# Kernel optimization log

Hardware: AMD Instinct MI355X
Metric: run time of the kernel (lower is better)

The kernel has to match this reference:

```python
import jax, jax.numpy as jnp
import numpy as np

FILTERS = [1, 3, 7, 9]
BN_EPS = 1e-5


def _conv1d(x, w, b):
    # x: [B, C, L], w: [O, I, F] (torch Conv1d layout), 'same' padding for odd F
    pad = (w.shape[-1] - 1) // 2
    y = jax.lax.conv_general_dilated(
        x, w, window_strides=(1,), padding=[(pad, pad)],
        dimension_numbers=("NCH", "OIH", "NCH"))
    return y + b[None, :, None]


def _bn_elu(x, gamma, beta):
    # BatchNorm1d in training mode: biased batch stats over (batch, length)
    m = jnp.mean(x, axis=(0, 2), keepdims=True)
    v = jnp.var(x, axis=(0, 2), keepdims=True)
    xn = (x - m) * jax.lax.rsqrt(v + BN_EPS)
    return jax.nn.elu(xn * gamma[None, :, None] + beta[None, :, None])


def setup_inputs() -> dict:
    key = jax.random.key(0)
    ks = jax.random.split(key, 32)
    b, h, l, lk, dk = 8, 8, 1024, 1024, 64
    inp = {
        "Q": jax.random.normal(ks[0], (b, h, l, dk), jnp.float32),
        "K": jax.random.normal(ks[1], (b, h, lk, dk), jnp.float32),
        "V": jax.random.normal(ks[2], (b, h, lk, dk), jnp.float32),
        "W_pq": jax.random.normal(ks[3], (1, dk), jnp.float32) * 0.1,
        "W_bq": jax.random.normal(ks[4], (dk, 1), jnp.float32) * 0.1,
        "W_bk": jax.random.normal(ks[5], (dk, 1), jnp.float32) * 0.1,
        "bn_g": jax.random.uniform(ks[6], (h,), jnp.float32, 0.5, 1.5),
        "bn_b": jax.random.normal(ks[7], (h,), jnp.float32) * 0.1,
        "attn_mask": jnp.ones((1,), dtype=bool),
    }
    for i, f in enumerate(FILTERS):
        s = 1.0 / np.sqrt(h * f)
        inp[f"cq_w{i}"] = jax.random.normal(ks[8 + i], (h, h, f), jnp.float32) * s
        inp[f"cq_b{i}"] = jax.random.normal(ks[12 + i], (h,), jnp.float32) * 0.05
        inp[f"ck_w{i}"] = jax.random.normal(ks[16 + i], (h, h, f), jnp.float32) * s
        inp[f"ck_b{i}"] = jax.random.normal(ks[20 + i], (h,), jnp.float32) * 0.05
    return inp


def reference(Q, K, V, W_pq, W_bq, W_bk,
              cq_w0, cq_b0, cq_w1, cq_b1, cq_w2, cq_b2, cq_w3, cq_b3,
              ck_w0, ck_b0, ck_w1, ck_b1, ck_w2, ck_b2, ck_w3, ck_b3,
              bn_g, bn_b, attn_mask):
    b, h, l, dk = Q.shape
    lk = K.shape[2]
    nf = len(FILTERS)
    # proj_q applied to BOTH Q and K (proj_k is dead in the original code)
    q = jnp.einsum("bhld,d->bhl", Q, W_pq[0])  # [b,h,l]
    k = jnp.einsum("bhld,d->bhl", K, W_pq[0])  # [b,h,lk]
    cq = [(cq_w0, cq_b0), (cq_w1, cq_b1), (cq_w2, cq_b2), (cq_w3, cq_b3)]
    ck = [(ck_w0, ck_b0), (ck_w1, ck_b1), (ck_w2, ck_b2), (ck_w3, ck_b3)]
    Q_l = [_bn_elu(_conv1d(q, w, bb), bn_g, bn_b) for w, bb in cq]
    K_l = [_bn_elu(_conv1d(k, w, bb), bn_g, bn_b) for w, bb in ck]
    # replicate torch.cat(dim=0) + reshape(b,h,nf*len) flat-order semantics
    Q_p = jnp.concatenate(Q_l, axis=0).reshape(b, h, nf * l)    # [b,h,4l]
    K_p = jnp.concatenate(K_l, axis=0).reshape(b, h, nf * lk)   # [b,h,4lk]
    Qt = jax.lax.top_k(Q_p, l)[0]                               # [b,h,l]
    Km = jnp.mean(K_p.reshape(b, h, nf, lk), axis=2)            # [b,h,lk]
    Kt = jax.lax.top_k(Km, lk)[0]                               # descending sort
    Qb = Qt[..., None] * W_bq[:, 0]                             # [b,h,l,dk]
    Kb = Kt[..., None] * W_bk[:, 0]                             # [b,h,lk,dk]
    scores = jnp.einsum("bhqd,bhkd->bhqk", Qb, Kb) / np.float32(np.sqrt(dk))
    attn = jax.nn.softmax(scores, axis=-1)
    context = jnp.einsum("bhqk,bhkd->bhqd", attn, V)
    return context, attn
```

## Files before the change

kernel.cpp:

```cpp
#include <hip/hip_runtime.h>
#include <hip/hip_bf16.h>
#include <math.h>

namespace {
constexpr int PROJ_OFF = 0;
constexpr int CONV_OFF = 131072;
constexpr int PS_OFF   = 655360;
constexpr int PSS_OFF  = 657408;
constexpr int QT_OFF   = 659456;
constexpr int KT_OFF   = 724992;

typedef short bf16x8 __attribute__((ext_vector_type(8)));
typedef float f32x4 __attribute__((ext_vector_type(4)));

union BF8 {
  bf16x8 v;
  short s[8];
};

__global__ __launch_bounds__(256) void proj_kernel(
    const float* __restrict__ Q, const float* __restrict__ K,
    const float* __restrict__ Wpq, float* __restrict__ proj) {
  __shared__ float wsh[64];
  const int tid = threadIdx.x;
  if (tid < 64) wsh[tid] = Wpq[tid];
  __syncthreads();
  const int row = blockIdx.x * 256 + tid;
  const float* src = (row < 65536) ? (Q + (size_t)row * 64)
                                   : (K + (size_t)(row - 65536) * 64);
  float acc = 0.f;
#pragma unroll
  for (int j = 0; j < 16; ++j) {
    const float4 v = *(const float4*)(src + j * 4);
    acc = fmaf(v.x, wsh[j * 4 + 0], acc);
    acc = fmaf(v.y, wsh[j * 4 + 1], acc);
    acc = fmaf(v.z, wsh[j * 4 + 2], acc);
    acc = fmaf(v.w, wsh[j * 4 + 3], acc);
  }
  proj[row] = acc;
}

template <int F>
__device__ void conv_body(const float* __restrict__ xs,
                          const float* __restrict__ wsm,
                          const float* __restrict__ bsm,
                          float* __restrict__ outp, int tid, int lq,
                          float accs[8]) {
  constexpr int pad = (F - 1) / 2;
#pragma unroll
  for (int j = 0; j < 8; ++j) {
    float acc = bsm[j];
#pragma unroll
    for (int c = 0; c < 8; ++c) {
      const float* xrow = &xs[c * 264 + tid + 4 - pad];
      const float* wrow = &wsm[(j * 8 + c) * F];
#pragma unroll
      for (int f = 0; f < F; ++f) acc = fmaf(xrow[f], wrow[f], acc);
    }
    outp[j * 1024 + lq * 256 + tid] = acc;
    accs[j] = acc;
  }
}

__global__ __launch_bounds__(256) void conv_kernel(
    const float* __restrict__ proj,
    const float* __restrict__ wq0, const float* __restrict__ bq0,
    const float* __restrict__ wq1, const float* __restrict__ bq1,
    const float* __restrict__ wq2, const float* __restrict__ bq2,
    const float* __restrict__ wq3, const float* __restrict__ bq3,
    const float* __restrict__ wk0, const float* __restrict__ bk0,
    const float* __restrict__ wk1, const float* __restrict__ bk1,
    const float* __restrict__ wk2, const float* __restrict__ bk2,
    const float* __restrict__ wk3, const float* __restrict__ bk3,
    float* __restrict__ conv, float* __restrict__ psum,
    float* __restrict__ psumsq) {
  __shared__ float xs[8 * 264];
  __shared__ float wsm[8 * 8 * 9];
  __shared__ float bsm[8];
  __shared__ float redS[8][4], redSS[8][4];
  const int tid = threadIdx.x;
  const int blk = blockIdx.x;
  const int path = blk >> 7, fi = (blk >> 5) & 3, bb = (blk >> 2) & 7;
  const int lq = blk & 3;
  const int F = (0x9731 >> (fi * 4)) & 0xF;
  const float* wp;
  const float* bp;
  if (path == 0) {
    wp = fi == 0 ? wq0 : fi == 1 ? wq1 : fi == 2 ? wq2 : wq3;
    bp = fi == 0 ? bq0 : fi == 1 ? bq1 : fi == 2 ? bq2 : bq3;
  } else {
    wp = fi == 0 ? wk0 : fi == 1 ? wk1 : fi == 2 ? wk2 : wk3;
    bp = fi == 0 ? bk0 : fi == 1 ? bk1 : fi == 2 ? bk2 : bk3;
  }
  const float* pb = proj + path * 65536 + bb * 8192;
  for (int e = tid; e < 8 * 264; e += 256) {
    const int c = e / 264, pos = e - c * 264;
    const int gl = lq * 256 + pos - 4;
    xs[e] = (gl >= 0 && gl < 1024) ? pb[c * 1024 + gl] : 0.f;
  }
  for (int e = tid; e < 64 * F; e += 256) wsm[e] = wp[e];
  if (tid < 8) bsm[tid] = bp[tid];
  __syncthreads();
  float* outp = conv + ((size_t)(path * 4 + fi) * 8 + bb) * 8192;
  float accs[8];
  if (fi == 0)
    conv_body<1>(xs, wsm, bsm, outp, tid, lq, accs);
  else if (fi == 1)
    conv_body<3>(xs, wsm, bsm, outp, tid, lq, accs);
  else if (fi == 2)
    conv_body<7>(xs, wsm, bsm, outp, tid, lq, accs);
  else
    conv_body<9>(xs, wsm, bsm, outp, tid, lq, accs);
  const int lane = tid & 63, wv = tid >> 6;
#pragma unroll
  for (int j = 0; j < 8; ++j) {
    float sv = accs[j], qv = accs[j] * accs[j];
#pragma unroll
    for (int mm = 32; mm >= 1; mm >>= 1) {
      sv += __shfl_xor(sv, mm, 64);
      qv += __shfl_xor(qv, mm, 64);
    }
    if (lane == 0) {
      redS[j][wv] = sv;
      redSS[j][wv] = qv;
    }
  }
  __syncthreads();
  if (tid < 16) {
    const int j = tid & 7;
    const bool wantss = tid >= 8;
    const float* rr = wantss ? &redSS[j][0] : &redS[j][0];
    const float tot = rr[0] + rr[1] + rr[2] + rr[3];
    float* dst = wantss ? psumsq : psum;
    dst[((path * 4 + fi) * 8 + j) * 32 + bb * 4 + lq] = tot;
  }
}

__device__ inline float bn_elu(float v, float mean, float rstd, float g,
                               float be) {
  const float x = (v - mean) * rstd * g + be;
  return x > 0.f ? x : expm1f(x);
}

__device__ inline void cswap(float& a, float& b, bool up) {
  const float mx = fmaxf(a, b), mn = fminf(a, b);
  a = up ? mx : mn;
  b = up ? mn : mx;
}

__device__ inline void shfl_pass(float v[4], int t, int m, bool up) {
  const bool keepmax = (up == ((t & m) == 0));
#pragma unroll
  for (int e = 0; e < 4; ++e) {
    const float p = __shfl_xor(v[e], m, 64);
    v[e] = keepmax ? fmaxf(v[e], p) : fminf(v[e], p);
  }
}

__device__ inline void lds_pass(float v[4], float* s, int t, int jq, bool up) {
  *(float4*)&s[4 * t] = make_float4(v[0], v[1], v[2], v[3]);
  __syncthreads();
  const int pt = t ^ jq;
  const bool keepmax = (up == ((t & jq) == 0));
  const float4 p = *(const float4*)&s[4 * pt];
  v[0] = keepmax ? fmaxf(v[0], p.x) : fminf(v[0], p.x);
  v[1] = keepmax ? fmaxf(v[1], p.y) : fminf(v[1], p.y);
  v[2] = keepmax ? fmaxf(v[2], p.z) : fminf(v[2], p.z);
  v[3] = keepmax ? fmaxf(v[3], p.w) : fminf(v[3], p.w);
  __syncthreads();
}

__device__ inline void reg_tail(float v[4], int t, bool up) {
#pragma unroll
  for (int m = 32; m >= 1; m >>= 1) shfl_pass(v, t, m, up);
  cswap(v[0], v[2], up);
  cswap(v[1], v[3], up);
  cswap(v[0], v[1], up);
  cswap(v[2], v[3], up);
}

__device__ inline void sort1024(float v[4], float* s, int t) {
  cswap(v[0], v[1], true);
  cswap(v[2], v[3], false);
#pragma unroll
  for (int k = 4; k <= 256; k <<= 1) {
    const bool up = ((t & (k >> 2)) == 0);
    for (int m = k >> 3; m >= 1; m >>= 1) shfl_pass(v, t, m, up);
    cswap(v[0], v[2], up);
    cswap(v[1], v[3], up);
    cswap(v[0], v[1], up);
    cswap(v[2], v[3], up);
  }
  {
    const bool up = ((t & 128) == 0);
    lds_pass(v, s, t, 64, up);
    reg_tail(v, t, up);
  }
  lds_pass(v, s, t, 128, true);
  lds_pass(v, s, t, 64, true);
  reg_tail(v, t, true);
}

__device__ inline void bmerge1024(float v[4], float* s, int t) {
  lds_pass(v, s, t, 128, true);
  lds_pass(v, s, t, 64, true);
  reg_tail(v, t, true);
}

__global__ __launch_bounds__(256) void sortmerge_kernel(
    const float* __restrict__ conv, const float* __restrict__ psum,
    const float* __restrict__ psumsq, const float* __restrict__ bng,
    const float* __restrict__ bnb, float* __restrict__ Qt,
    float* __restrict__ Kt) {
  __shared__ float s[1024];
  __shared__ float sred[8];
  __shared__ float cm[4], cr[4];
  const int t = threadIdx.x, blk = blockIdx.x;
  const bool isQ = blk < 64;
  const int row = isQ ? blk : blk - 64;
  const int hp = row & 7;
  const int fi = row >> 4;
  const int bb = ((row >> 3) & 1) * 4 + (hp >> 1);
  const int chbase = (isQ ? 0 : 32) + fi * 8 + (hp & 1) * 4;
  if (t < 8) {
    const float* src = (t < 4) ? psum : psumsq;
    const int ch = chbase + (t & 3);
    float a = 0.f;
    for (int i = 0; i < 32; ++i) a += src[ch * 32 + i];
    sred[t] = a;
  }
  __syncthreads();
  if (t < 4) {
    const float mean = sred[t] * (1.f / 8192.f);
    const float var = sred[4 + t] * (1.f / 8192.f) - mean * mean;
    cm[t] = mean;
    cr[t] = rsqrtf(fmaxf(var, 0.f) + 1e-5f);
  }
  __syncthreads();
  if (isQ) {
    const float* base = conv + (size_t)(fi * 8 + bb) * 8192;
    float c0[4], c1[4], c2[4], c3[4];
#pragma unroll
    for (int jc = 0; jc < 4; ++jc) {
      float* v = jc == 0 ? c0 : jc == 1 ? c1 : jc == 2 ? c2 : c3;
      const int hh = (hp & 1) * 4 + jc;
      const float mean = cm[jc], rstd = cr[jc];
      const float g = bng[hh], be = bnb[hh];
      const float4 x = *(const float4*)&base[hh * 1024 + 4 * t];
      v[0] = bn_elu(x.x, mean, rstd, g, be);
      v[1] = bn_elu(x.y, mean, rstd, g, be);
      v[2] = bn_elu(x.z, mean, rstd, g, be);
      v[3] = bn_elu(x.w, mean, rstd, g, be);
      sort1024(v, s, t);
    }
    float a[4], b[4];
    *(float4*)&s[4 * t] = make_float4(c1[0], c1[1], c1[2], c1[3]);
    __syncthreads();
#pragma unroll
    for (int e = 0; e < 4; ++e) a[e] = fmaxf(c0[e], s[1023 - 4 * t - e]);
    __syncthreads();
    bmerge1024(a, s, t);
    *(float4*)&s[4 * t] = make_float4(c3[0], c3[1], c3[2], c3[3]);
    __syncthreads();
#pragma unroll
    for (int e = 0; e < 4; ++e) b[e] = fmaxf(c2[e], s[1023 - 4 * t - e]);
    __syncthreads();
    bmerge1024(b, s, t);
    *(float4*)&s[4 * t] = make_float4(b[0], b[1], b[2], b[3]);
    __syncthreads();
#pragma unroll
    for (int e = 0; e < 4; ++e) a[e] = fmaxf(a[e], s[1023 - 4 * t - e]);
    __syncthreads();
    bmerge1024(a, s, t);
    *(float4*)&Qt[(size_t)row * 1024 + 4 * t] =
        make_float4(a[0], a[1], a[2], a[3]);
  } else {
    float v[4];
    float sum0 = 0.f, sum1 = 0.f, sum2 = 0.f, sum3 = 0.f;
#pragma unroll
    for (int j = 0; j < 4; ++j) {
      const int hh = (hp & 1) * 4 + j;
      const float mean = cm[j], rstd = cr[j];
      const float g = bng[hh], be = bnb[hh];
      const float4 x = *(const float4*)&conv[(size_t)(4 + fi) * 64 * 1024 +
                                             (size_t)bb * 8192 + hh * 1024 +
                                             4 * t];
      sum0 += bn_elu(x.x, mean, rstd, g, be);
      sum1 += bn_elu(x.y, mean, rstd, g, be);
      sum2 += bn_elu(x.z, mean, rstd, g, be);
      sum3 += bn_elu(x.w, mean, rstd, g, be);
    }
    v[0] = sum0 * 0.25f;
    v[1] = sum1 * 0.25f;
    v[2] = sum2 * 0.25f;
    v[3] = sum3 * 0.25f;
    sort1024(v, s, t);
    *(float4*)&Kt[(size_t)row * 1024 + 4 * t] =
        make_float4(v[0], v[1], v[2], v[3]);
  }
}

__global__ __launch_bounds__(256, 4) void attn5_kernel(
    const float* __restrict__ V, const float* __restrict__ Qt,
    const float* __restrict__ Kt, const float* __restrict__ Wbq,
    const float* __restrict__ Wbk, float* __restrict__ ctx,
    float* __restrict__ attn) {
  __shared__ float Kts[1024];
  __shared__ float sq[64], mq[64], rz[64];
  __shared__ short Vhi[2][8 * 64 * 8];
  __shared__ short Vlo[2][8 * 64 * 8];
  const int tid = threadIdx.x;
  const int b = blockIdx.x;
  const int bh = ((b & 7) << 3) | ((b >> 3) & 7);
  const int qt = b >> 6;
  const int qbase = qt * 64;
  const int lane0 = tid & 63;
  float cval;
  {
    float d = Wbq[lane0] * Wbk[lane0];
#pragma unroll
    for (int mm = 32; mm >= 1; mm >>= 1) d += __shfl_xor(d, mm, 64);
    cval = d * 0.125f;
  }
  const float* Ktg = Kt + (size_t)bh * 1024;
  for (int t = tid; t < 1024; t += 256) Kts[t] = Ktg[t];
  const float kHi = Ktg[0], kLo = Ktg[1023];
  if (tid < 64) {
    const float s = cval * Qt[(size_t)bh * 1024 + qbase + tid];
    sq[tid] = s;
    mq[tid] = fmaxf(s * kHi, s * kLo);
  }
  __syncthreads();
  {
    const int row = tid >> 2, qtr = tid & 3;
    const float s = sq[row], m = mq[row];
    float z = 0.f;
    const int k0 = qtr * 256;
    for (int k = 0; k < 256; ++k) z += __expf(fmaf(s, Kts[k0 + k], -m));
    z += __shfl_xor(z, 1, 64);
    z += __shfl_xor(z, 2, 64);
    if (qtr == 0) rz[row] = 1.f / z;
  }
  __syncthreads();

  const int wv = tid >> 6, l = tid & 63;
  const int l15 = l & 15, l4 = l >> 4;
  const int q = wv * 16 + l15;
  const float s = sq[q], m = mq[q], r = rz[q];
  f32x4 acc[4];
#pragma unroll
  for (int dt = 0; dt < 4; ++dt) acc[dt] = (f32x4){0.f, 0.f, 0.f, 0.f};

  const float* Vb = V + (size_t)bh * 65536;
  float* arow = attn + ((size_t)bh << 20) + (size_t)qbase * 1024;
  const int dV = tid & 63, kqV = tid >> 6;

  for (int ch = 0; ch < 16; ++ch) {
    const int kc = ch * 64;
    const int buf = ch & 1;
    float vreg[2][8];
#pragma unroll
    for (int g = 0; g < 2; ++g) {
      const int ko = kqV + g * 4;
      const float* vs = Vb + (size_t)(kc + ko * 8) * 64 + dV;
#pragma unroll
      for (int i = 0; i < 8; ++i) vreg[g][i] = vs[i * 64];
    }
    bf16x8 ahi[2], alo[2];
#pragma unroll
    for (int ks = 0; ks < 2; ++ks) {
      const int kb = kc + ks * 32 + l4 * 8;
      const float4 kv0 = *(const float4*)&Kts[kb];
      const float4 kv1 = *(const float4*)&Kts[kb + 4];
      float e[8];
      e[0] = __expf(fmaf(s, kv0.x, -m)) * r;
      e[1] = __expf(fmaf(s, kv0.y, -m)) * r;
      e[2] = __expf(fmaf(s, kv0.z, -m)) * r;
      e[3] = __expf(fmaf(s, kv0.w, -m)) * r;
      e[4] = __expf(fmaf(s, kv1.x, -m)) * r;
      e[5] = __expf(fmaf(s, kv1.y, -m)) * r;
      e[6] = __expf(fmaf(s, kv1.z, -m)) * r;
      e[7] = __expf(fmaf(s, kv1.w, -m)) * r;
      float* ag = arow + (size_t)q * 1024 + kb;
      *(float4*)ag = make_float4(e[0], e[1], e[2], e[3]);
      *(float4*)(ag + 4) = make_float4(e[4], e[5], e[6], e[7]);
      BF8 H, L;
#pragma unroll
      for (int i = 0; i < 8; ++i) {
        const __hip_bfloat16 hb = __float2bfloat16(e[i]);
        H.s[i] = __bfloat16_as_short(hb);
        L.s[i] =
            __bfloat16_as_short(__float2bfloat16(e[i] - __bfloat162float(hb)));
      }
      ahi[ks] = H.v;
      alo[ks] = L.v;
    }
#pragma unroll
    for (int g = 0; g < 2; ++g) {
      const int ko = kqV + g * 4;
      BF8 H, L;
#pragma unroll
      for (int i = 0; i < 8; ++i) {
        const float f = vreg[g][i];
        const __hip_bfloat16 hb = __float2bfloat16(f);
        H.s[i] = __bfloat16_as_short(hb);
        L.s[i] =
            __bfloat16_as_short(__float2bfloat16(f - __bfloat162float(hb)));
      }
      *(bf16x8*)&Vhi[buf][(ko * 64 + dV) * 8] = H.v;
      *(bf16x8*)&Vlo[buf][(ko * 64 + dV) * 8] = L.v;
    }
    __syncthreads();
#pragma unroll
    for (int ks = 0; ks < 2; ++ks) {
      const int ko = ks * 4 + l4;
#pragma unroll
      for (int dt = 0; dt < 4; ++dt) {
        const bf16x8 bhv =
            *(const bf16x8*)&Vhi[buf][(ko * 64 + dt * 16 + l15) * 8];
        const bf16x8 blv =
            *(const bf16x8*)&Vlo[buf][(ko * 64 + dt * 16 + l15) * 8];
        acc[dt] = __builtin_amdgcn_mfma_f32_16x16x32_bf16(ahi[ks], bhv,
                                                          acc[dt], 0, 0, 0);
        acc[dt] = __builtin_amdgcn_mfma_f32_16x16x32_bf16(ahi[ks], blv,
                                                          acc[dt], 0, 0, 0);
        acc[dt] = __builtin_amdgcn_mfma_f32_16x16x32_bf16(alo[ks], bhv,
                                                          acc[dt], 0, 0, 0);
      }
    }
  }
  float* cb = ctx + ((size_t)bh * 1024 + qbase + wv * 16 + l4 * 4) * 64 + l15;
#pragma unroll
  for (int dt = 0; dt < 4; ++dt)
#pragma unroll
    for (int rr = 0; rr < 4; ++rr) cb[(size_t)rr * 64 + dt * 16] = acc[dt][rr];
}

}

extern "C" void kernel_launch(void* const* d_in, const int* in_sizes, int n_in,
                              void* d_out, int out_size, void* d_ws,
                              size_t ws_size, hipStream_t stream) {
  const float* Q = (const float*)d_in[0];
  const float* K = (const float*)d_in[1];
  const float* V = (const float*)d_in[2];
  const float* Wpq = (const float*)d_in[3];
  const float* Wbq = (const float*)d_in[4];
  const float* Wbk = (const float*)d_in[5];
  const float* bng = (const float*)d_in[6];
  const float* bnb = (const float*)d_in[7];
  const float* cqw[4] = {(const float*)d_in[9], (const float*)d_in[13],
                         (const float*)d_in[17], (const float*)d_in[21]};
  const float* cqb[4] = {(const float*)d_in[10], (const float*)d_in[14],
                         (const float*)d_in[18], (const float*)d_in[22]};
  const float* ckw[4] = {(const float*)d_in[11], (const float*)d_in[15],
                         (const float*)d_in[19], (const float*)d_in[23]};
  const float* ckb[4] = {(const float*)d_in[12], (const float*)d_in[16],
                         (const float*)d_in[20], (const float*)d_in[24]};

  float* ws = (float*)d_ws;
  float* proj = ws + PROJ_OFF;
  float* conv = ws + CONV_OFF;
  float* psum = ws + PS_OFF;
  float* psumsq = ws + PSS_OFF;
  float* Qtp = ws + QT_OFF;
  float* Ktp = ws + KT_OFF;
  float* ctx = (float*)d_out;
  float* attn = ctx + (size_t)8 * 8 * 1024 * 64;

  proj_kernel<<<512, 256, 0, stream>>>(Q, K, Wpq, proj);
  conv_kernel<<<256, 256, 0, stream>>>(
      proj, cqw[0], cqb[0], cqw[1], cqb[1], cqw[2], cqb[2], cqw[3], cqb[3],
      ckw[0], ckb[0], ckw[1], ckb[1], ckw[2], ckb[2], ckw[3], ckb[3], conv,
      psum, psumsq);
  sortmerge_kernel<<<128, 256, 0, stream>>>(conv, psum, psumsq, bng, bnb, Qtp,
                                            Ktp);
  attn5_kernel<<<1024, 256, 0, stream>>>(V, Qtp, Ktp, Wbq, Wbk, ctx, attn);
}
```

Baseline: 119.8 us.

## Process 128 query rows per block to reuse V conversion across two tiles

The attention kernel now handles 128 queries per block instead of 64, and the grid is halved. Each wave computes two 16-row MFMA tiles that share the same bf16 hi/lo V tiles in LDS, so V loads and splits are amortised over twice as many queries. The softmax normaliser is folded into the exponent as -m-log(z), which removes a multiply per element. The attn row stores are moved after a custom lgkmcnt barrier so they overlap with the MFMA phase. In exchange, register pressure roughly doubles (launch bounds drop to 2 blocks per SM), and only 512 blocks remain to fill the GPU.

```diff
diff --git a/kernel.cpp b/kernel.cpp
--- a/kernel.cpp
+++ b/kernel.cpp
@@ -17,6 +17,13 @@
   bf16x8 v;
   short s[8];
 };
+
+__device__ inline void lgkm_barrier() {
+  __builtin_amdgcn_sched_barrier(0);
+  asm volatile("s_waitcnt lgkmcnt(0)" ::: "memory");
+  __builtin_amdgcn_s_barrier();
+  __builtin_amdgcn_sched_barrier(0);
+}
 
 __global__ __launch_bounds__(256) void proj_kernel(
     const float* __restrict__ Q, const float* __restrict__ K,
@@ -300,20 +307,20 @@
   }
 }
 
-__global__ __launch_bounds__(256, 4) void attn5_kernel(
+__global__ __launch_bounds__(256, 2) void attn6_kernel(
     const float* __restrict__ V, const float* __restrict__ Qt,
     const float* __restrict__ Kt, const float* __restrict__ Wbq,
     const float* __restrict__ Wbk, float* __restrict__ ctx,
     float* __restrict__ attn) {
   __shared__ float Kts[1024];
-  __shared__ float sq[64], mq[64], rz[64];
+  __shared__ float sq[128], cz[128];
   __shared__ short Vhi[2][8 * 64 * 8];
   __shared__ short Vlo[2][8 * 64 * 8];
   const int tid = threadIdx.x;
   const int b = blockIdx.x;
   const int bh = ((b & 7) << 3) | ((b >> 3) & 7);
   const int qt = b >> 6;
-  const int qbase = qt * 64;
+  const int qbase = qt * 128;
   const int lane0 = tid & 63;
   float cval;
   {
@@ -325,31 +332,37 @@
   const float* Ktg = Kt + (size_t)bh * 1024;
   for (int t = tid; t < 1024; t += 256) Kts[t] = Ktg[t];
   const float kHi = Ktg[0], kLo = Ktg[1023];
-  if (tid < 64) {
+  __shared__ float msh[128];
+  if (tid < 128) {
     const float s = cval * Qt[(size_t)bh * 1024 + qbase + tid];
     sq[tid] = s;
-    mq[tid] = fmaxf(s * kHi, s * kLo);
+    msh[tid] = fmaxf(s * kHi, s * kLo);
   }
   __syncthreads();
   {
-    const int row = tid >> 2, qtr = tid & 3;
-    const float s = sq[row], m = mq[row];
+    const int row = tid >> 1, half = tid & 1;
+    const float s = sq[row], m = msh[row];
+    const int k0 = half * 512;
     float z = 0.f;
-    const int k0 = qtr * 256;
-    for (int k = 0; k < 256; ++k) z += __expf(fmaf(s, Kts[k0 + k], -m));
+    for (int k = 0; k < 512; ++k) z += __expf(fmaf(s, Kts[k0 + k], -m));
     z += __shfl_xor(z, 1, 64);
-    z += __shfl_xor(z, 2, 64);
-    if (qtr == 0) rz[row] = 1.f / z;
+    if (half == 0) cz[row] = -m - __logf(z);
   }
   __syncthreads();
 
   const int wv = tid >> 6, l = tid & 63;
   const int l15 = l & 15, l4 = l >> 4;
-  const int q = wv * 16 + l15;
-  const float s = sq[q], m = mq[q], r = rz[q];
-  f32x4 acc[4];
-#pragma unroll
-  for (int dt = 0; dt < 4; ++dt) acc[dt] = (f32x4){0.f, 0.f, 0.f, 0.f};
+  float s_[2], c_[2];
+#pragma unroll
+  for (int t = 0; t < 2; ++t) {
+    s_[t] = sq[wv * 32 + t * 16 + l15];
+    c_[t] = cz[wv * 32 + t * 16 + l15];
+  }
+  f32x4 acc[2][4];
+#pragma unroll
+  for (int t = 0; t < 2; ++t)
+#pragma unroll
+    for (int dt = 0; dt < 4; ++dt) acc[t][dt] = (f32x4){0.f, 0.f, 0.f, 0.f};
 
   const float* Vb = V + (size_t)bh * 65536;
   float* arow = attn + ((size_t)bh << 20) + (size_t)qbase * 1024;
@@ -366,34 +379,38 @@
 #pragma unroll
       for (int i = 0; i < 8; ++i) vreg[g][i] = vs[i * 64];
     }
-    bf16x8 ahi[2], alo[2];
+    bf16x8 ahi[2][2], alo[2][2];
+    float4 est[2][2][2];
 #pragma unroll
     for (int ks = 0; ks < 2; ++ks) {
       const int kb = kc + ks * 32 + l4 * 8;
       const float4 kv0 = *(const float4*)&Kts[kb];
       const float4 kv1 = *(const float4*)&Kts[kb + 4];
-      float e[8];
-      e[0] = __expf(fmaf(s, kv0.x, -m)) * r;
-      e[1] = __expf(fmaf(s, kv0.y, -m)) * r;
-      e[2] = __expf(fmaf(s, kv0.z, -m)) * r;
-      e[3] = __expf(fmaf(s, kv0.w, -m)) * r;
-      e[4] = __expf(fmaf(s, kv1.x, -m)) * r;
-      e[5] = __expf(fmaf(s, kv1.y, -m)) * r;
-      e[6] = __expf(fmaf(s, kv1.z, -m)) * r;
-      e[7] = __expf(fmaf(s, kv1.w, -m)) * r;
-      float* ag = arow + (size_t)q * 1024 + kb;
-      *(float4*)ag = make_float4(e[0], e[1], e[2], e[3]);
-      *(float4*)(ag + 4) = make_float4(e[4], e[5], e[6], e[7]);
-      BF8 H, L;
-#pragma unroll
-      for (int i = 0; i < 8; ++i) {
-        const __hip_bfloat16 hb = __float2bfloat16(e[i]);
-        H.s[i] = __bfloat16_as_short(hb);
-        L.s[i] =
-            __bfloat16_as_short(__float2bfloat16(e[i] - __bfloat162float(hb)));
+#pragma unroll
+      for (int t = 0; t < 2; ++t) {
+        const float s = s_[t], c = c_[t];
+        float e[8];
+        e[0] = __expf(fmaf(s, kv0.x, c));
+        e[1] = __expf(fmaf(s, kv0.y, c));
+        e[2] = __expf(fmaf(s, kv0.z, c));
+        e[3] = __expf(fmaf(s, kv0.w, c));
+        e[4] = __expf(fmaf(s, kv1.x, c));
+        e[5] = __expf(fmaf(s, kv1.y, c));
+        e[6] = __expf(fmaf(s, kv1.z, c));
+        e[7] = __expf(fmaf(s, kv1.w, c));
+        est[t][ks][0] = make_float4(e[0], e[1], e[2], e[3]);
+        est[t][ks][1] = make_float4(e[4], e[5], e[6], e[7]);
+        BF8 H, L;
+#pragma unroll
+        for (int i = 0; i < 8; ++i) {
+          const __hip_bfloat16 hb = __float2bfloat16(e[i]);
+          H.s[i] = __bfloat16_as_short(hb);
+          L.s[i] = __bfloat16_as_short(
+              __float2bfloat16(e[i] - __bfloat162float(hb)));
+        }
+        ahi[t][ks] = H.v;
+        alo[t][ks] = L.v;
       }
-      ahi[ks] = H.v;
-      alo[ks] = L.v;
     }
 #pragma unroll
     for (int g = 0; g < 2; ++g) {
@@ -410,7 +427,17 @@
       *(bf16x8*)&Vhi[buf][(ko * 64 + dV) * 8] = H.v;
       *(bf16x8*)&Vlo[buf][(ko * 64 + dV) * 8] = L.v;
     }
-    __syncthreads();
+    lgkm_barrier();
+#pragma unroll
+    for (int t = 0; t < 2; ++t) {
+      const int q = wv * 32 + t * 16 + l15;
+#pragma unroll
+      for (int ks = 0; ks < 2; ++ks) {
+        float* ag = arow + (size_t)q * 1024 + kc + ks * 32 + l4 * 8;
+        *(float4*)ag = est[t][ks][0];
+        *(float4*)(ag + 4) = est[t][ks][1];
+      }
+    }
 #pragma unroll
     for (int ks = 0; ks < 2; ++ks) {
       const int ko = ks * 4 + l4;
@@ -420,20 +447,29 @@
             *(const bf16x8*)&Vhi[buf][(ko * 64 + dt * 16 + l15) * 8];
         const bf16x8 blv =
             *(const bf16x8*)&Vlo[buf][(ko * 64 + dt * 16 + l15) * 8];
-        acc[dt] = __builtin_amdgcn_mfma_f32_16x16x32_bf16(ahi[ks], bhv,
-                                                          acc[dt], 0, 0, 0);
-        acc[dt] = __builtin_amdgcn_mfma_f32_16x16x32_bf16(ahi[ks], blv,
-                                                          acc[dt], 0, 0, 0);
-        acc[dt] = __builtin_amdgcn_mfma_f32_16x16x32_bf16(alo[ks], bhv,
-                                                          acc[dt], 0, 0, 0);
+#pragma unroll
+        for (int t = 0; t < 2; ++t) {
+          acc[t][dt] = __builtin_amdgcn_mfma_f32_16x16x32_bf16(
+              ahi[t][ks], bhv, acc[t][dt], 0, 0, 0);
+          acc[t][dt] = __builtin_amdgcn_mfma_f32_16x16x32_bf16(
+              ahi[t][ks], blv, acc[t][dt], 0, 0, 0);
+          acc[t][dt] = __builtin_amdgcn_mfma_f32_16x16x32_bf16(
+              alo[t][ks], bhv, acc[t][dt], 0, 0, 0);
+        }
       }
     }
   }
-  float* cb = ctx + ((size_t)bh * 1024 + qbase + wv * 16 + l4 * 4) * 64 + l15;
-#pragma unroll
-  for (int dt = 0; dt < 4; ++dt)
-#pragma unroll
-    for (int rr = 0; rr < 4; ++rr) cb[(size_t)rr * 64 + dt * 16] = acc[dt][rr];
+#pragma unroll
+  for (int t = 0; t < 2; ++t) {
+    float* cb = ctx +
+                ((size_t)bh * 1024 + qbase + wv * 32 + t * 16 + l4 * 4) * 64 +
+                l15;
+#pragma unroll
+    for (int dt = 0; dt < 4; ++dt)
+#pragma unroll
+      for (int rr = 0; rr < 4; ++rr)
+        cb[(size_t)rr * 64 + dt * 16] = acc[t][dt][rr];
+  }
 }
 
 }
@@ -475,5 +511,5 @@
       psum, psumsq);
   sortmerge_kernel<<<128, 256, 0, stream>>>(conv, psum, psumsq, bng, bnb, Qtp,
                                             Ktp);
-  attn5_kernel<<<1024, 256, 0, stream>>>(V, Qtp, Ktp, Wbq, Wbk, ctx, attn);
-}
+  attn6_kernel<<<512, 256, 0, stream>>>(V, Qtp, Ktp, Wbq, Wbk, ctx, attn);
+}
```

Measured after the change: 129.6 us. +8.2%, slower.

## Prefetch next V chunk across barrier and fold softmax normalizer into exponent

Applied to the files above, without the earlier changes.

The attention kernel now loads the next 64-row V chunk into registers right after the chunk barrier, so global loads overlap the MFMA work instead of stalling at the top of each iteration. It replaces __syncthreads with a barrier that waits only on LDS counters, which keeps outstanding global loads and stores in flight. The attn probability stores are deferred until after the barrier. Softmax normalization is folded into the exponent as -m-log(z), which removes a multiply per element at a small cost in rounding accuracy.

```diff
diff --git a/kernel.cpp b/kernel.cpp
--- a/kernel.cpp
+++ b/kernel.cpp
@@ -17,6 +17,13 @@
   bf16x8 v;
   short s[8];
 };
+
+__device__ inline void lgkm_barrier() {
+  __builtin_amdgcn_sched_barrier(0);
+  asm volatile("s_waitcnt lgkmcnt(0)" ::: "memory");
+  __builtin_amdgcn_s_barrier();
+  __builtin_amdgcn_sched_barrier(0);
+}
 
 __global__ __launch_bounds__(256) void proj_kernel(
     const float* __restrict__ Q, const float* __restrict__ K,
@@ -300,13 +307,13 @@
   }
 }
 
-__global__ __launch_bounds__(256, 4) void attn5_kernel(
+__global__ __launch_bounds__(256, 4) void attn7_kernel(
     const float* __restrict__ V, const float* __restrict__ Qt,
     const float* __restrict__ Kt, const float* __restrict__ Wbq,
     const float* __restrict__ Wbk, float* __restrict__ ctx,
     float* __restrict__ attn) {
   __shared__ float Kts[1024];
-  __shared__ float sq[64], mq[64], rz[64];
+  __shared__ float sq[64], cz[64], msh[64];
   __shared__ short Vhi[2][8 * 64 * 8];
   __shared__ short Vlo[2][8 * 64 * 8];
   const int tid = threadIdx.x;
@@ -328,25 +335,25 @@
   if (tid < 64) {
     const float s = cval * Qt[(size_t)bh * 1024 + qbase + tid];
     sq[tid] = s;
-    mq[tid] = fmaxf(s * kHi, s * kLo);
+    msh[tid] = fmaxf(s * kHi, s * kLo);
   }
   __syncthreads();
   {
     const int row = tid >> 2, qtr = tid & 3;
-    const float s = sq[row], m = mq[row];
+    const float s = sq[row], m = msh[row];
     float z = 0.f;
     const int k0 = qtr * 256;
     for (int k = 0; k < 256; ++k) z += __expf(fmaf(s, Kts[k0 + k], -m));
     z += __shfl_xor(z, 1, 64);
     z += __shfl_xor(z, 2, 64);
-    if (qtr == 0) rz[row] = 1.f / z;
+    if (qtr == 0) cz[row] = -m - __logf(z);
   }
   __syncthreads();
 
   const int wv = tid >> 6, l = tid & 63;
   const int l15 = l & 15, l4 = l >> 4;
   const int q = wv * 16 + l15;
-  const float s = sq[q], m = mq[q], r = rz[q];
+  const float s = sq[q], c = cz[q];
   f32x4 acc[4];
 #pragma unroll
   for (int dt = 0; dt < 4; ++dt) acc[dt] = (f32x4){0.f, 0.f, 0.f, 0.f};
@@ -355,35 +362,35 @@
   float* arow = attn + ((size_t)bh << 20) + (size_t)qbase * 1024;
   const int dV = tid & 63, kqV = tid >> 6;
 
+  float vreg[2][8];
+#pragma unroll
+  for (int g = 0; g < 2; ++g) {
+    const float* vs = Vb + (size_t)((kqV + g * 4) * 8) * 64 + dV;
+#pragma unroll
+    for (int i = 0; i < 8; ++i) vreg[g][i] = vs[i * 64];
+  }
+
   for (int ch = 0; ch < 16; ++ch) {
     const int kc = ch * 64;
     const int buf = ch & 1;
-    float vreg[2][8];
-#pragma unroll
-    for (int g = 0; g < 2; ++g) {
-      const int ko = kqV + g * 4;
-      const float* vs = Vb + (size_t)(kc + ko * 8) * 64 + dV;
-#pragma unroll
-      for (int i = 0; i < 8; ++i) vreg[g][i] = vs[i * 64];
-    }
     bf16x8 ahi[2], alo[2];
+    float4 est[2][2];
 #pragma unroll
     for (int ks = 0; ks < 2; ++ks) {
       const int kb = kc + ks * 32 + l4 * 8;
       const float4 kv0 = *(const float4*)&Kts[kb];
       const float4 kv1 = *(const float4*)&Kts[kb + 4];
       float e[8];
-      e[0] = __expf(fmaf(s, kv0.x, -m)) * r;
-      e[1] = __expf(fmaf(s, kv0.y, -m)) * r;
-      e[2] = __expf(fmaf(s, kv0.z, -m)) * r;
-      e[3] = __expf(fmaf(s, kv0.w, -m)) * r;
-      e[4] = __expf(fmaf(s, kv1.x, -m)) * r;
-      e[5] = __expf(fmaf(s, kv1.y, -m)) * r;
-      e[6] = __expf(fmaf(s, kv1.z, -m)) * r;
-      e[7] = __expf(fmaf(s, kv1.w, -m)) * r;
-      float* ag = arow + (size_t)q * 1024 + kb;
-      *(float4*)ag = make_float4(e[0], e[1], e[2], e[3]);
-      *(float4*)(ag + 4) = make_float4(e[4], e[5], e[6], e[7]);
+      e[0] = __expf(fmaf(s, kv0.x, c));
+      e[1] = __expf(fmaf(s, kv0.y, c));
+      e[2] = __expf(fmaf(s, kv0.z, c));
+      e[3] = __expf(fmaf(s, kv0.w, c));
+      e[4] = __expf(fmaf(s, kv1.x, c));
+      e[5] = __expf(fmaf(s, kv1.y, c));
+      e[6] = __expf(fmaf(s, kv1.z, c));
+      e[7] = __expf(fmaf(s, kv1.w, c));
+      est[ks][0] = make_float4(e[0], e[1], e[2], e[3]);
+      est[ks][1] = make_float4(e[4], e[5], e[6], e[7]);
       BF8 H, L;
 #pragma unroll
       for (int i = 0; i < 8; ++i) {
@@ -410,7 +417,22 @@
       *(bf16x8*)&Vhi[buf][(ko * 64 + dV) * 8] = H.v;
       *(bf16x8*)&Vlo[buf][(ko * 64 + dV) * 8] = L.v;
     }
-    __syncthreads();
+    lgkm_barrier();
+    if (ch < 15) {
+#pragma unroll
+      for (int g = 0; g < 2; ++g) {
+        const float* vs =
+            Vb + (size_t)(kc + 64 + (kqV + g * 4) * 8) * 64 + dV;
+#pragma unroll
+        for (int i = 0; i < 8; ++i) vreg[g][i] = vs[i * 64];
+      }
+    }
+#pragma unroll
+    for (int ks = 0; ks < 2; ++ks) {
+      float* ag = arow + (size_t)q * 1024 + kc + ks * 32 + l4 * 8;
+      *(float4*)ag = est[ks][0];
+      *(float4*)(ag + 4) = est[ks][1];
+    }
 #pragma unroll
     for (int ks = 0; ks < 2; ++ks) {
       const int ko = ks * 4 + l4;
@@ -475,5 +497,5 @@
       psum, psumsq);
   sortmerge_kernel<<<128, 256, 0, stream>>>(conv, psum, psumsq, bng, bnb, Qtp,
                                             Ktp);
-  attn5_kernel<<<1024, 256, 0, stream>>>(V, Qtp, Ktp, Wbq, Wbk, ctx, attn);
-}
+  attn7_kernel<<<1024, 256, 0, stream>>>(V, Qtp, Ktp, Wbq, Wbk, ctx, attn);
+}
```

After: 122.4 us. +2.1%, slower.

## Sort each 1024-row within a single wavefront and merge Q sorts in parallel

Applied to the files above, without the earlier changes.

Replaces the block-wide bitonic sort, which does LDS exchanges with barriers, with a per-wavefront sort that keeps 16 values per lane and uses only shuffles and in-register compare-swaps. For Q rows the four channel sorts now run concurrently in four waves and are merged in a tree through shared memory. K rows are packed four per block, so the grid drops from 128 to 80 blocks. This removes most barriers and serial sort phases, at the cost of higher register pressure and fewer active blocks.

```diff
diff --git a/kernel.cpp b/kernel.cpp
--- a/kernel.cpp
+++ b/kernel.cpp
@@ -148,155 +148,173 @@
   b = up ? mn : mx;
 }
 
-__device__ inline void shfl_pass(float v[4], int t, int m, bool up) {
-  const bool keepmax = (up == ((t & m) == 0));
-#pragma unroll
-  for (int e = 0; e < 4; ++e) {
-    const float p = __shfl_xor(v[e], m, 64);
-    v[e] = keepmax ? fmaxf(v[e], p) : fminf(v[e], p);
-  }
-}
-
-__device__ inline void lds_pass(float v[4], float* s, int t, int jq, bool up) {
-  *(float4*)&s[4 * t] = make_float4(v[0], v[1], v[2], v[3]);
-  __syncthreads();
-  const int pt = t ^ jq;
-  const bool keepmax = (up == ((t & jq) == 0));
-  const float4 p = *(const float4*)&s[4 * pt];
-  v[0] = keepmax ? fmaxf(v[0], p.x) : fminf(v[0], p.x);
-  v[1] = keepmax ? fmaxf(v[1], p.y) : fminf(v[1], p.y);
-  v[2] = keepmax ? fmaxf(v[2], p.z) : fminf(v[2], p.z);
-  v[3] = keepmax ? fmaxf(v[3], p.w) : fminf(v[3], p.w);
-  __syncthreads();
-}
-
-__device__ inline void reg_tail(float v[4], int t, bool up) {
-#pragma unroll
-  for (int m = 32; m >= 1; m >>= 1) shfl_pass(v, t, m, up);
-  cswap(v[0], v[2], up);
-  cswap(v[1], v[3], up);
-  cswap(v[0], v[1], up);
-  cswap(v[2], v[3], up);
-}
-
-__device__ inline void sort1024(float v[4], float* s, int t) {
-  cswap(v[0], v[1], true);
-  cswap(v[2], v[3], false);
-#pragma unroll
-  for (int k = 4; k <= 256; k <<= 1) {
-    const bool up = ((t & (k >> 2)) == 0);
-    for (int m = k >> 3; m >= 1; m >>= 1) shfl_pass(v, t, m, up);
-    cswap(v[0], v[2], up);
-    cswap(v[1], v[3], up);
-    cswap(v[0], v[1], up);
-    cswap(v[2], v[3], up);
-  }
-  {
-    const bool up = ((t & 128) == 0);
-    lds_pass(v, s, t, 64, up);
-    reg_tail(v, t, up);
-  }
-  lds_pass(v, s, t, 128, true);
-  lds_pass(v, s, t, 64, true);
-  reg_tail(v, t, true);
-}
-
-__device__ inline void bmerge1024(float v[4], float* s, int t) {
-  lds_pass(v, s, t, 128, true);
-  lds_pass(v, s, t, 64, true);
-  reg_tail(v, t, true);
-}
-
-__global__ __launch_bounds__(256) void sortmerge_kernel(
+__device__ inline void wsort1024(float v[16], int lane) {
+#pragma unroll
+  for (int k = 2; k <= 1024; k <<= 1) {
+#pragma unroll
+    for (int j = 512; j >= 16; j >>= 1) {
+      if (j <= (k >> 1)) {
+        const int lj = j >> 4;
+        const bool up = ((lane & (k >> 4)) == 0);
+        const bool keep = (up == ((lane & lj) == 0));
+#pragma unroll
+        for (int e = 0; e < 16; ++e) {
+          const float p = __shfl_xor(v[e], lj, 64);
+          v[e] = keep ? fmaxf(v[e], p) : fminf(v[e], p);
+        }
+      }
+    }
+#pragma unroll
+    for (int j = 8; j >= 1; j >>= 1) {
+      if (j <= (k >> 1)) {
+#pragma unroll
+        for (int e = 0; e < 16; ++e) {
+          if ((e & j) == 0) {
+            bool up;
+            if (k >= 32)
+              up = ((lane & (k >> 4)) == 0);
+            else if (k == 16)
+              up = ((lane & 1) == 0);
+            else
+              up = ((e & k) == 0);
+            cswap(v[e], v[e ^ j], up);
+          }
+        }
+      }
+    }
+  }
+}
+
+__device__ inline void wmerge1024(float v[16], int lane) {
+#pragma unroll
+  for (int lj = 32; lj >= 1; lj >>= 1) {
+    const bool keep = ((lane & lj) == 0);
+#pragma unroll
+    for (int e = 0; e < 16; ++e) {
+      const float p = __shfl_xor(v[e], lj, 64);
+      v[e] = keep ? fmaxf(v[e], p) : fminf(v[e], p);
+    }
+  }
+#pragma unroll
+  for (int j = 8; j >= 1; j >>= 1)
+#pragma unroll
+    for (int e = 0; e < 16; ++e)
+      if ((e & j) == 0) cswap(v[e], v[e ^ j], true);
+}
+
+__global__ __launch_bounds__(256) void sortmerge2_kernel(
     const float* __restrict__ conv, const float* __restrict__ psum,
     const float* __restrict__ psumsq, const float* __restrict__ bng,
     const float* __restrict__ bnb, float* __restrict__ Qt,
     float* __restrict__ Kt) {
-  __shared__ float s[1024];
-  __shared__ float sred[8];
-  __shared__ float cm[4], cr[4];
-  const int t = threadIdx.x, blk = blockIdx.x;
-  const bool isQ = blk < 64;
-  const int row = isQ ? blk : blk - 64;
-  const int hp = row & 7;
-  const int fi = row >> 4;
-  const int bb = ((row >> 3) & 1) * 4 + (hp >> 1);
-  const int chbase = (isQ ? 0 : 32) + fi * 8 + (hp & 1) * 4;
-  if (t < 8) {
-    const float* src = (t < 4) ? psum : psumsq;
-    const int ch = chbase + (t & 3);
-    float a = 0.f;
-    for (int i = 0; i < 32; ++i) a += src[ch * 32 + i];
-    sred[t] = a;
-  }
-  __syncthreads();
-  if (t < 4) {
-    const float mean = sred[t] * (1.f / 8192.f);
-    const float var = sred[4 + t] * (1.f / 8192.f) - mean * mean;
-    cm[t] = mean;
-    cr[t] = rsqrtf(fmaxf(var, 0.f) + 1e-5f);
-  }
-  __syncthreads();
-  if (isQ) {
-    const float* base = conv + (size_t)(fi * 8 + bb) * 8192;
-    float c0[4], c1[4], c2[4], c3[4];
-#pragma unroll
-    for (int jc = 0; jc < 4; ++jc) {
-      float* v = jc == 0 ? c0 : jc == 1 ? c1 : jc == 2 ? c2 : c3;
-      const int hh = (hp & 1) * 4 + jc;
-      const float mean = cm[jc], rstd = cr[jc];
-      const float g = bng[hh], be = bnb[hh];
-      const float4 x = *(const float4*)&base[hh * 1024 + 4 * t];
-      v[0] = bn_elu(x.x, mean, rstd, g, be);
-      v[1] = bn_elu(x.y, mean, rstd, g, be);
-      v[2] = bn_elu(x.z, mean, rstd, g, be);
-      v[3] = bn_elu(x.w, mean, rstd, g, be);
-      sort1024(v, s, t);
-    }
-    float a[4], b[4];
-    *(float4*)&s[4 * t] = make_float4(c1[0], c1[1], c1[2], c1[3]);
+  __shared__ float s1[1024];
+  __shared__ float s2[1024];
+  const int tid = threadIdx.x, blk = blockIdx.x;
+  const int wv = tid >> 6, l = tid & 63;
+  float v[16];
+  if (blk < 64) {
+    const int row = blk;
+    const int hp = row & 7, fi = row >> 4;
+    const int bb = ((row >> 3) & 1) * 4 + (hp >> 1);
+    const int hh = (hp & 1) * 4 + wv;
+    const int ch = fi * 8 + hh;
+    float sval = 0.f;
+    if (l < 2) {
+      const float* src = (l == 0) ? psum : psumsq;
+#pragma unroll
+      for (int i = 0; i < 32; ++i) sval += src[ch * 32 + i];
+    }
+    const float mean = __shfl(sval, 0, 64) * (1.f / 8192.f);
+    const float msq = __shfl(sval, 1, 64) * (1.f / 8192.f);
+    const float rstd = rsqrtf(fmaxf(msq - mean * mean, 0.f) + 1e-5f);
+    const float g = bng[hh], be = bnb[hh];
+    const float* base = conv + (size_t)(fi * 8 + bb) * 8192 + hh * 1024;
+#pragma unroll
+    for (int j = 0; j < 4; ++j) {
+      const float4 x = *(const float4*)&base[l * 16 + j * 4];
+      v[j * 4 + 0] = bn_elu(x.x, mean, rstd, g, be);
+      v[j * 4 + 1] = bn_elu(x.y, mean, rstd, g, be);
+      v[j * 4 + 2] = bn_elu(x.z, mean, rstd, g, be);
+      v[j * 4 + 3] = bn_elu(x.w, mean, rstd, g, be);
+    }
+    wsort1024(v, l);
+    if (wv == 1)
+#pragma unroll
+      for (int e = 0; e < 16; ++e) s1[l * 16 + e] = v[e];
+    if (wv == 3)
+#pragma unroll
+      for (int e = 0; e < 16; ++e) s2[l * 16 + e] = v[e];
     __syncthreads();
-#pragma unroll
-    for (int e = 0; e < 4; ++e) a[e] = fmaxf(c0[e], s[1023 - 4 * t - e]);
+    if (wv == 0) {
+#pragma unroll
+      for (int e = 0; e < 16; ++e)
+        v[e] = fmaxf(v[e], s1[1023 - (l * 16 + e)]);
+      wmerge1024(v, l);
+    } else if (wv == 2) {
+#pragma unroll
+      for (int e = 0; e < 16; ++e)
+        v[e] = fmaxf(v[e], s2[1023 - (l * 16 + e)]);
+      wmerge1024(v, l);
+#pragma unroll
+      for (int e = 0; e < 16; ++e) s2[l * 16 + e] = v[e];
+    }
     __syncthreads();
-    bmerge1024(a, s, t);
-    *(float4*)&s[4 * t] = make_float4(c3[0], c3[1], c3[2], c3[3]);
-    __syncthreads();
-#pragma unroll
-    for (int e = 0; e < 4; ++e) b[e] = fmaxf(c2[e], s[1023 - 4 * t - e]);
-    __syncthreads();
-    bmerge1024(b, s, t);
-    *(float4*)&s[4 * t] = make_float4(b[0], b[1], b[2], b[3]);
-    __syncthreads();
-#pragma unroll
-    for (int e = 0; e < 4; ++e) a[e] = fmaxf(a[e], s[1023 - 4 * t - e]);
-    __syncthreads();
-    bmerge1024(a, s, t);
-    *(float4*)&Qt[(size_t)row * 1024 + 4 * t] =
-        make_float4(a[0], a[1], a[2], a[3]);
+    if (wv == 0) {
+#pragma unroll
+      for (int e = 0; e < 16; ++e)
+        v[e] = fmaxf(v[e], s2[1023 - (l * 16 + e)]);
+      wmerge1024(v, l);
+      float* qd = Qt + (size_t)row * 1024 + l * 16;
+#pragma unroll
+      for (int j = 0; j < 4; ++j)
+        *(float4*)&qd[j * 4] =
+            make_float4(v[j * 4], v[j * 4 + 1], v[j * 4 + 2], v[j * 4 + 3]);
+    }
   } else {
-    float v[4];
-    float sum0 = 0.f, sum1 = 0.f, sum2 = 0.f, sum3 = 0.f;
+    const int row = (blk - 64) * 4 + wv;
+    const int hp = row & 7, fi = row >> 4;
+    const int bb = ((row >> 3) & 1) * 4 + (hp >> 1);
+    const int chk = 32 + fi * 8 + (hp & 1) * 4;
+    float sval = 0.f;
+    if (l < 8) {
+      const float* src = (l < 4) ? psum : psumsq;
+      const int ch = chk + (l & 3);
+#pragma unroll
+      for (int i = 0; i < 32; ++i) sval += src[ch * 32 + i];
+    }
+    float cm[4], cr[4];
+#pragma unroll
+    for (int j = 0; j < 4; ++j) {
+      const float mean = __shfl(sval, j, 64) * (1.f / 8192.f);
+      const float msq = __shfl(sval, j + 4, 64) * (1.f / 8192.f);
+      cm[j] = mean;
+      cr[j] = rsqrtf(fmaxf(msq - mean * mean, 0.f) + 1e-5f);
+    }
+#pragma unroll
+    for (int e = 0; e < 16; ++e) v[e] = 0.f;
 #pragma unroll
     for (int j = 0; j < 4; ++j) {
       const int hh = (hp & 1) * 4 + j;
-      const float mean = cm[j], rstd = cr[j];
       const float g = bng[hh], be = bnb[hh];
-      const float4 x = *(const float4*)&conv[(size_t)(4 + fi) * 64 * 1024 +
-                                             (size_t)bb * 8192 + hh * 1024 +
-                                             4 * t];
-      sum0 += bn_elu(x.x, mean, rstd, g, be);
-      sum1 += bn_elu(x.y, mean, rstd, g, be);
-      sum2 += bn_elu(x.z, mean, rstd, g, be);
-      sum3 += bn_elu(x.w, mean, rstd, g, be);
-    }
-    v[0] = sum0 * 0.25f;
-    v[1] = sum1 * 0.25f;
-    v[2] = sum2 * 0.25f;
-    v[3] = sum3 * 0.25f;
-    sort1024(v, s, t);
-    *(float4*)&Kt[(size_t)row * 1024 + 4 * t] =
-        make_float4(v[0], v[1], v[2], v[3]);
+      const float* base =
+          conv + (size_t)(4 + fi) * 64 * 1024 + (size_t)bb * 8192 + hh * 1024;
+#pragma unroll
+      for (int jj = 0; jj < 4; ++jj) {
+        const float4 x = *(const float4*)&base[l * 16 + jj * 4];
+        v[jj * 4 + 0] += bn_elu(x.x, cm[j], cr[j], g, be);
+        v[jj * 4 + 1] += bn_elu(x.y, cm[j], cr[j], g, be);
+        v[jj * 4 + 2] += bn_elu(x.z, cm[j], cr[j], g, be);
+        v[jj * 4 + 3] += bn_elu(x.w, cm[j], cr[j], g, be);
+      }
+    }
+#pragma unroll
+    for (int e = 0; e < 16; ++e) v[e] *= 0.25f;
+    wsort1024(v, l);
+    float* kd = Kt + (size_t)row * 1024 + l * 16;
+#pragma unroll
+    for (int j = 0; j < 4; ++j)
+      *(float4*)&kd[j * 4] =
+          make_float4(v[j * 4], v[j * 4 + 1], v[j * 4 + 2], v[j * 4 + 3]);
   }
 }
 
@@ -473,7 +491,7 @@
       proj, cqw[0], cqb[0], cqw[1], cqb[1], cqw[2], cqb[2], cqw[3], cqb[3],
       ckw[0], ckb[0], ckw[1], ckb[1], ckw[2], ckb[2], ckw[3], ckb[3], conv,
       psum, psumsq);
-  sortmerge_kernel<<<128, 256, 0, stream>>>(conv, psum, psumsq, bng, bnb, Qtp,
+  sortmerge2_kernel<<<80, 256, 0, stream>>>(conv, psum, psumsq, bng, bnb, Qtp,
                                             Ktp);
   attn5_kernel<<<1024, 256, 0, stream>>>(V, Qtp, Ktp, Wbq, Wbk, ctx, attn);
 }
```

Measured after the change: 119.2 us. Within noise of the previous version (-0.5%).
